# Kernel tuning notes

Hardware: AMD Instinct MI355X
Metric: run time of the kernel (lower is better)

The kernel has to match this reference:

```python
import jax, jax.numpy as jnp
from jax import lax
import numpy as np

H = 768          # BERT-base hidden size
NLAB = 2         # labelnum
T = NLAB + 2     # CRF tagset incl START/STOP (NCRF++ convention)
START = NLAB     # index 2
STOP = NLAB + 1  # index 3


def setup_inputs() -> dict:
    key = jax.random.key(0)
    ks = jax.random.split(key, 8)
    B, S1 = 64, 513  # S1 = 1 (CLS) + 512 content tokens
    emb = jax.random.normal(ks[0], (B, S1, H), dtype=jnp.float32)
    answer_seq_label = jax.random.randint(ks[1], (B, S1), 0, NLAB)
    IsQA = jax.random.randint(ks[2], (B,), 0, 2)
    fc2_W = jax.random.normal(ks[3], (2, H), dtype=jnp.float32) * 0.02
    fc2_b = jnp.zeros((2,), dtype=jnp.float32)
    crf_W = jax.random.normal(ks[4], (T, H), dtype=jnp.float32) * 0.02
    crf_b = jnp.zeros((T,), dtype=jnp.float32)
    transitions = jax.random.normal(ks[5], (T, T), dtype=jnp.float32) * 0.1
    return {"emb": emb, "answer_seq_label": answer_seq_label, "IsQA": IsQA,
            "fc2_W": fc2_W, "fc2_b": fc2_b, "crf_W": crf_W, "crf_b": crf_b,
            "transitions": transitions}


def _crf_log_partition(feats, trans):
    # feats [B,S,T]; linear-chain forward algorithm (log-sum-exp scan)
    alpha0 = feats[:, 0] + trans[START][None]           # [B,T]
    def step(alpha, feat_t):
        # alpha[b,prev] + trans[prev,cur] -> logsumexp over prev
        new = jax.nn.logsumexp(alpha[:, :, None] + trans[None], axis=1) + feat_t
        return new, None
    alpha, _ = lax.scan(step, alpha0, jnp.swapaxes(feats[:, 1:], 0, 1))
    return jax.nn.logsumexp(alpha + trans[:, STOP][None], axis=1)  # [B]


def _crf_gold_score(feats, tags, trans):
    # feats [B,S,T], tags [B,S]
    emit = jnp.take_along_axis(feats, tags[:, :, None], axis=2)[..., 0].sum(axis=1)
    tr = trans[tags[:, :-1], tags[:, 1:]].sum(axis=1)
    tr = tr + trans[START, tags[:, 0]] + trans[tags[:, -1], STOP]
    return emit + tr


def _crf_viterbi(feats, trans):
    # feats [B,S,T] -> best path [B,S]
    delta0 = feats[:, 0] + trans[START][None]
    def step(delta, feat_t):
        scores = delta[:, :, None] + trans[None]   # [B,prev,cur]
        bp = jnp.argmax(scores, axis=1)            # [B,T]
        return jnp.max(scores, axis=1) + feat_t, bp
    delta, bps = lax.scan(step, delta0, jnp.swapaxes(feats[:, 1:], 0, 1))  # bps [S-1,B,T]
    last_tag = jnp.argmax(delta + trans[:, STOP][None], axis=1)            # [B]
    def back(tag, bp_t):
        prev = jnp.take_along_axis(bp_t, tag[:, None], axis=1)[:, 0]
        return prev, prev
    _, path_prefix = lax.scan(back, last_tag, bps, reverse=True)           # [S-1,B]
    return jnp.concatenate([path_prefix, last_tag[None]], axis=0).T        # [B,S]


def reference(emb, answer_seq_label, IsQA, fc2_W, fc2_b, crf_W, crf_b, transitions):
    # CLS head + cross-entropy
    cls_emb = emb[:, 0]                              # [B,H]
    isqa_logits = cls_emb @ fc2_W.T + fc2_b          # [B,2]
    logp = jax.nn.log_softmax(isqa_logits, axis=-1)
    isqa_loss = -jnp.take_along_axis(logp, IsQA[:, None], axis=1).mean()
    isqa_pred = jnp.argmax(isqa_logits, axis=-1)[:, None]
    # CRF head (dropout = identity in eval); feats [B,S,T]
    feats = jnp.einsum('bsh,th->bst', emb[:, 1:], crf_W) + crf_b
    tags = answer_seq_label[:, 1:]
    Z = _crf_log_partition(feats, transitions)
    gold = _crf_gold_score(feats, tags, transitions)
    crf_loss = jnp.mean(Z - gold)
    crf_pred = _crf_viterbi(feats, transitions)
    return (isqa_pred, crf_pred, isqa_loss, crf_loss, tags, IsQA[:, None])
```

## Files before the change

kernel.cpp:

```cpp
#include <hip/hip_runtime.h>
#include <math.h>

#define B     64
#define S1    513
#define S     512
#define H     768
#define T     4
#define START 2
#define STOP  3

#define OUT_ISQA_PRED 0
#define OUT_CRF_PRED  64
#define OUT_ISQA_LOSS 32832
#define OUT_CRF_LOSS  32833
#define OUT_TAGS      32834
#define OUT_ISQA      65602

#define WS_FEATS  0
#define WS_LOGITS (B*S*T)
#define WS_ZG     (B*S*T + 2*B)
#define WS_CNT    (B*S*T + 3*B)
#define WS_FEATST 131280

template<int CTRL>
__device__ __forceinline__ float dppf(float x) {
    int v = __builtin_amdgcn_update_dpp(__builtin_bit_cast(int, x),
                                        __builtin_bit_cast(int, x),
                                        CTRL, 0xF, 0xF, false);
    return __builtin_bit_cast(float, v);
}
template<int CTRL>
__device__ __forceinline__ int dppi(int x) {
    return __builtin_amdgcn_update_dpp(x, x, CTRL, 0xF, 0xF, false);
}

__device__ __forceinline__ float lse4(float x0, float x1, float x2, float x3) {
    float m = fmaxf(fmaxf(x0, x1), fmaxf(x2, x3));
    return m + __logf(__expf(x0 - m) + __expf(x1 - m) +
                      __expf(x2 - m) + __expf(x3 - m));
}

__device__ __forceinline__ float wred(float a) {
    a += dppf<0xB1>(a); a += dppf<0x4E>(a);
    a += __shfl_xor(a, 4); a += __shfl_xor(a, 8);
    a += __shfl_xor(a, 16); a += __shfl_xor(a, 32);
    return a;
}

__device__ __forceinline__ float dot4(float4 e, float4 w) {
    return e.x * w.x + e.y * w.y + e.z * w.z + e.w * w.w;
}

__global__ __launch_bounds__(64) void feats_kernel(
    const float* __restrict__ emb,
    const float* __restrict__ crf_W, const float* __restrict__ crf_b,
    float* __restrict__ ws)
{
    if (blockIdx.x == 0 && threadIdx.x == 0)
        ((int*)ws)[WS_CNT] = 0;

    const int lane = threadIdx.x;
    const int r    = blockIdx.x * 64 + lane;
    const int b    = r >> 9;
    const int s    = (r & 511) + 1;

    const float4* __restrict__ src4 =
        (const float4*)emb + (size_t)(b * S1 + s) * (H / 4);
    const float4* __restrict__ W4 = (const float4*)crf_W;

    float a0 = 0.f, a1 = 0.f, a2 = 0.f, a3 = 0.f;
    #pragma unroll 8
    for (int k = 0; k < 192; ++k) {
        const float4 e  = src4[k];
        const float4 w0 = W4[0 * 192 + k];
        const float4 w1 = W4[1 * 192 + k];
        const float4 w2 = W4[2 * 192 + k];
        const float4 w3 = W4[3 * 192 + k];
        a0 += dot4(e, w0);
        a1 += dot4(e, w1);
        a2 += dot4(e, w2);
        a3 += dot4(e, w3);
    }

    const float v0 = a0 + crf_b[0];
    const float v1 = a1 + crf_b[1];
    const float v2 = a2 + crf_b[2];
    const float v3 = a3 + crf_b[3];

    float* __restrict__ fN = ws + WS_FEATS;
    float* __restrict__ fT = ws + WS_FEATST;
    ((float4*)fN)[b * S + (s - 1)] = make_float4(v0, v1, v2, v3);
    const int tb = b * 4 * S + (s - 1);
    fT[tb + 0 * S] = v0;
    fT[tb + 1 * S] = v1;
    fT[tb + 2 * S] = v2;
    fT[tb + 3 * S] = v3;
}

__device__ __forceinline__ unsigned int vstep(
    float& d, float fv,
    float tc0, float tc1, float tc2, float tc3, int sh8j)
{
    const float d0 = dppf<0x00>(d), d1 = dppf<0x55>(d);
    const float d2 = dppf<0xAA>(d), d3 = dppf<0xFF>(d);
    const float y0 = d0 + tc0, y1 = d1 + tc1;
    const float y2 = d2 + tc2, y3 = d3 + tc3;
    const float m01 = fmaxf(y0, y1), m23 = fmaxf(y2, y3);
    const int   i01 = (y1 > y0) ? 1 : 0;
    const int   i23 = (y3 > y2) ? 3 : 2;
    const int   bi  = (m23 > m01) ? i23 : i01;
    d = fmaxf(m01, m23) + fv;
    unsigned int mb = (unsigned int)bi << sh8j;
    unsigned int t1 = mb | (unsigned int)dppi<0xB1>((int)mb);
    return t1 | (unsigned int)dppi<0x4E>((int)t1);
}

__global__ __launch_bounds__(256) void crf_kernel(
    const int* __restrict__ ans, const int* __restrict__ isqa,
    const float* __restrict__ emb,
    const float* __restrict__ fc2_W, const float* __restrict__ fc2_b,
    const float* __restrict__ trans,
    float* __restrict__ ws, float* __restrict__ out)
{
    __shared__ float smemf[10784];
    __shared__ int isLast;
    const int tid = threadIdx.x;
    const int blk = blockIdx.x;

    if (blk < 64) {
        const int b = blk;
        float* sf  = smemf;
        float* C   = smemf + 2048;
        float* red = smemf + 3072;

        float tr[16];
        #pragma unroll
        for (int i = 0; i < 16; ++i) tr[i] = trans[i];

        {
            float4* sf4 = (float4*)sf;
            const float4* src4 = (const float4*)(ws + WS_FEATS) + b * 512;
            sf4[tid] = src4[tid];
            sf4[tid + 256] = src4[tid + 256];
        }

        if (tid < 128) {
            const int wv   = tid >> 6;
            const int lane = tid & 63;
            const float4* e4 = (const float4*)emb + (size_t)b * S1 * (H / 4);
            const float4* w4 = (const float4*)fc2_W + wv * 192;
            float acc = 0.f;
            #pragma unroll
            for (int k = 0; k < 3; ++k) {
                const float4 e = e4[lane + 64 * k];
                const float4 w = w4[lane + 64 * k];
                acc += dot4(e, w);
            }
            acc = wred(acc);
            if (lane == 0) {
                ws[WS_LOGITS + 2 * b + wv] = acc + fc2_b[wv];
                __threadfence();
            }
        }
        __syncthreads();

        float g = 0.f;
        #pragma unroll
        for (int u = 0; u < 2; ++u) {
            const int t   = 2 * tid + u;
            const int tag = ans[b * S1 + 1 + t];
            out[OUT_TAGS + b * S + t] = (float)tag;
            g += sf[t * 4 + tag];
            g += (t == 0) ? tr[START * 4 + tag] : tr[ans[b * S1 + t] * 4 + tag];
            if (t == S - 1) g += tr[tag * 4 + STOP];
        }
        #pragma unroll
        for (int m = 32; m; m >>= 1) g += __shfl_xor(g, m);
        if ((tid & 63) == 0) red[tid >> 6] = g;

        const int c  = tid >> 2;
        const int jr = tid & 3;
        const int t0 = c ? 8 * c : 1;
        float rl[4];
        #pragma unroll
        for (int i = 0; i < 4; ++i) rl[i] = tr[jr * 4 + i] + sf[t0 * 4 + i];
        for (int t = t0 + 1; t <= 8 * c + 7; ++t) {
            const float f0 = sf[t*4+0], f1 = sf[t*4+1], f2 = sf[t*4+2], f3 = sf[t*4+3];
            float nr[4];
            #pragma unroll
            for (int i = 0; i < 4; ++i)
                nr[i] = lse4(rl[0] + tr[0*4+i], rl[1] + tr[1*4+i],
                             rl[2] + tr[2*4+i], rl[3] + tr[3*4+i]);
            rl[0] = nr[0] + f0; rl[1] = nr[1] + f1;
            rl[2] = nr[2] + f2; rl[3] = nr[3] + f3;
        }
        ((float4*)C)[c * 4 + jr] = make_float4(rl[0], rl[1], rl[2], rl[3]);
        __syncthreads();

        for (int d = 1; d <= 32; d <<= 1) {
            const int cs = (c >= d) ? (c - d) : c;
            float4 ar = ((float4*)C)[cs * 4 + jr];
            float4 b0 = ((float4*)C)[c * 4 + 0];
            float4 b1 = ((float4*)C)[c * 4 + 1];
            float4 b2 = ((float4*)C)[c * 4 + 2];
            float4 b3 = ((float4*)C)[c * 4 + 3];
            __syncthreads();
            if (c >= d) {
                float4 nr;
                nr.x = lse4(ar.x + b0.x, ar.y + b1.x, ar.z + b2.x, ar.w + b3.x);
                nr.y = lse4(ar.x + b0.y, ar.y + b1.y, ar.z + b2.y, ar.w + b3.y);
                nr.z = lse4(ar.x + b0.z, ar.y + b1.z, ar.z + b2.z, ar.w + b3.z);
                nr.w = lse4(ar.x + b0.w, ar.y + b1.w, ar.z + b2.w, ar.w + b3.w);
                ((float4*)C)[c * 4 + jr] = nr;
            }
            __syncthreads();
        }

        if (tid == 0) {
            const float gold = red[0] + red[1] + red[2] + red[3];
            float a0k[4];
            #pragma unroll
            for (int k = 0; k < 4; ++k) a0k[k] = sf[k] + tr[START * 4 + k];
            const float* P = C + 63 * 16;
            float aN[4];
            #pragma unroll
            for (int i = 0; i < 4; ++i)
                aN[i] = lse4(a0k[0] + P[0*4+i], a0k[1] + P[1*4+i],
                             a0k[2] + P[2*4+i], a0k[3] + P[3*4+i]);
            const float Z = lse4(aN[0] + tr[0*4+STOP], aN[1] + tr[1*4+STOP],
                                 aN[2] + tr[2*4+STOP], aN[3] + tr[3*4+STOP]);
            ws[WS_ZG + b] = Z - gold;
            out[OUT_ISQA + b] = (float)isqa[b];
            __threadfence();
            const int old = atomicAdd((int*)ws + WS_CNT, 1);
            isLast = (old == 63);
        }
        __syncthreads();

        if (isLast && tid < 64) {
            __threadfence();
            const float zg = ws[WS_ZG + tid];
            const float l0 = ws[WS_LOGITS + tid * 2 + 0];
            const float l1 = ws[WS_LOGITS + tid * 2 + 1];
            const float m  = fmaxf(l0, l1);
            const float lse = m + __logf(__expf(l0 - m) + __expf(l1 - m));
            const int   y   = isqa[tid];
            const float li  = lse - (y ? l1 : l0);
            float s1 = zg, s2 = li;
            #pragma unroll
            for (int d = 32; d; d >>= 1) {
                s1 += __shfl_xor(s1, d);
                s2 += __shfl_xor(s2, d);
            }
            out[OUT_ISQA_PRED + tid] = (l1 > l0) ? 1.0f : 0.0f;
            if (tid == 0) {
                out[OUT_CRF_LOSS]  = s1 * (1.0f / 64.0f);
                out[OUT_ISQA_LOSS] = s2 * (1.0f / 64.0f);
            }
        }
    } else {
        const int bv = blk - 64;
        float* sfT = smemf;
        unsigned int* bpw = (unsigned int*)(smemf + 8208);
        {
            float4* d4 = (float4*)sfT;
            const float4* s4 = (const float4*)(ws + WS_FEATST) + bv * 4 * 512;
            #pragma unroll
            for (int n = 0; n < 8; ++n) d4[tid + 256 * n] = s4[tid + 256 * n];
        }
        if (tid < 4) ((float4*)(sfT + 8192))[tid & 3] =
            make_float4(0.f, 0.f, 0.f, 0.f);
        __syncthreads();

        const int w    = tid >> 6;
        const int lane = tid & 63;
        const int j    = lane & 3;
        const int b    = bv * 4 + w;
        const int sh8j = 8 * j;

        const float tc0 = trans[0*4+j], tc1 = trans[1*4+j];
        const float tc2 = trans[2*4+j], tc3 = trans[3*4+j];
        const float tSj = trans[START*4+j];
        const float tjs = trans[j*4 + STOP];

        const float4* colT4 = (const float4*)(sfT + w * 2048 + j * 512);
        uint4* bpq = (uint4*)(bpw + w * 512);

        float4 A  = colT4[0];
        float4 Bq = colT4[1];
        float4 B2 = colT4[2];
        float d = A.x + tSj;
        {
            const unsigned int W1 = vstep(d, A.y, tc0, tc1, tc2, tc3, sh8j);
            const unsigned int W2 = vstep(d, A.z, tc0, tc1, tc2, tc3, sh8j);
            const unsigned int W3 = vstep(d, A.w, tc0, tc1, tc2, tc3, sh8j);
            if (lane == 0) bpq[0] = make_uint4(0x03020100u, W1, W2, W3);
        }
        for (int g = 1; g < 128; ++g) {
            const float4 Cq = colT4[g + 2];
            const unsigned int W0 = vstep(d, Bq.x, tc0, tc1, tc2, tc3, sh8j);
            const unsigned int W1 = vstep(d, Bq.y, tc0, tc1, tc2, tc3, sh8j);
            const unsigned int W2 = vstep(d, Bq.z, tc0, tc1, tc2, tc3, sh8j);
            const unsigned int W3 = vstep(d, Bq.w, tc0, tc1, tc2, tc3, sh8j);
            if (lane == 0) bpq[g] = make_uint4(W0, W1, W2, W3);
            Bq = B2; B2 = Cq;
        }

        const float vj = d + tjs;
        const float z0 = dppf<0x00>(vj), z1 = dppf<0x55>(vj);
        const float z2 = dppf<0xAA>(vj), z3 = dppf<0xFF>(vj);
        float m01 = z0; unsigned int i01 = 0;
        if (z1 > m01) { m01 = z1; i01 = 1; }
        float m23 = z2; unsigned int i23 = 2;
        if (z3 > m23) { m23 = z3; i23 = 3; }
        const unsigned int lt = (m23 > m01) ? i23 : i01;

        __syncthreads();

        const uint4 wv0 = bpq[lane * 2 + 0];
        const uint4 wv1 = bpq[lane * 2 + 1];
        unsigned int wk[8] = {wv0.x, wv0.y, wv0.z, wv0.w, wv1.x, wv1.y, wv1.z, wv1.w};
        unsigned int G = wk[7];
        #pragma unroll
        for (int k = 6; k >= 0; --k)
            G = __builtin_amdgcn_perm(0u, wk[k], G);
        unsigned int Sm = G;
        #pragma unroll
        for (int dd = 1; dd < 64; dd <<= 1) {
            const int srcl = lane + dd;
            const unsigned int oth = __shfl(Sm, (srcl < 64) ? srcl : 63);
            if (srcl < 64) Sm = __builtin_amdgcn_perm(0u, Sm, oth);
        }
        unsigned int emap = __shfl(Sm, (lane < 63) ? lane + 1 : 63);
        if (lane == 63) emap = 0x03020100u;
        unsigned int cur = (emap >> (8 * lt)) & 3u;

        float tg[8];
        tg[7] = (float)cur;
        #pragma unroll
        for (int k = 7; k >= 1; --k) {
            cur = (wk[k] >> (8 * cur)) & 3u;
            tg[k - 1] = (float)cur;
        }
        float4* op = (float4*)(out + OUT_CRF_PRED + b * S + lane * 8);
        op[0] = make_float4(tg[0], tg[1], tg[2], tg[3]);
        op[1] = make_float4(tg[4], tg[5], tg[6], tg[7]);
    }
}

extern "C" void kernel_launch(void* const* d_in, const int* in_sizes, int n_in,
                              void* d_out, int out_size, void* d_ws, size_t ws_size,
                              hipStream_t stream)
{
    const float* emb    = (const float*)d_in[0];
    const int*   ans    = (const int*)d_in[1];
    const int*   isqa   = (const int*)d_in[2];
    const float* fc2_W  = (const float*)d_in[3];
    const float* fc2_b  = (const float*)d_in[4];
    const float* crf_W  = (const float*)d_in[5];
    const float* crf_b  = (const float*)d_in[6];
    const float* trans  = (const float*)d_in[7];
    float* out = (float*)d_out;
    float* ws  = (float*)d_ws;

    feats_kernel<<<512, 64, 0, stream>>>(emb, crf_W, crf_b, ws);
    crf_kernel<<<80, 256, 0, stream>>>(ans, isqa, emb, fc2_W, fc2_b, trans, ws, out);
}
```

Baseline: 224.3 us.

## Stage embedding tiles through LDS with coalesced loads and split-K reduction

Restructures the feats projection kernel. Before, each thread streamed a whole 768-float row alone, giving strided, uncoalesced global loads. Now 256 threads cooperatively load 64-row by 16-float4 chunks into double-buffered, padded LDS, with crf_W cached in LDS. Each row's dot products are split across four thread groups and combined through shared memory. This aims for coalesced HBM reads and more memory-level parallelism, at the cost of extra LDS traffic and a barrier per chunk.

```diff
diff --git a/kernel.cpp b/kernel.cpp
--- a/kernel.cpp
+++ b/kernel.cpp
@@ -22,6 +22,11 @@
 #define WS_CNT    (B*S*T + 3*B)
 #define WS_FEATST 131280
 
+#define RB   64
+#define KC   16
+#define NC   12
+#define RS   17
+
 template<int CTRL>
 __device__ __forceinline__ float dppf(float x) {
     int v = __builtin_amdgcn_update_dpp(__builtin_bit_cast(int, x),
@@ -51,50 +56,96 @@
     return e.x * w.x + e.y * w.y + e.z * w.z + e.w * w.w;
 }
 
-__global__ __launch_bounds__(64) void feats_kernel(
+__global__ __launch_bounds__(256) void feats_kernel(
     const float* __restrict__ emb,
     const float* __restrict__ crf_W, const float* __restrict__ crf_b,
     float* __restrict__ ws)
 {
-    if (blockIdx.x == 0 && threadIdx.x == 0)
-        ((int*)ws)[WS_CNT] = 0;
-
-    const int lane = threadIdx.x;
-    const int r    = blockIdx.x * 64 + lane;
-    const int b    = r >> 9;
-    const int s    = (r & 511) + 1;
-
-    const float4* __restrict__ src4 =
-        (const float4*)emb + (size_t)(b * S1 + s) * (H / 4);
-    const float4* __restrict__ W4 = (const float4*)crf_W;
+    __shared__ float4 wlds[4 * 192];
+    __shared__ float4 buf[2][RB * RS];
+    __shared__ float4 red[3][RB];
+
+    const int tid = threadIdx.x;
+    const int blk = blockIdx.x;
+    if (blk == 0 && tid == 0) ((int*)ws)[WS_CNT] = 0;
+
+    {
+        const float4* W4 = (const float4*)crf_W;
+        wlds[tid]       = W4[tid];
+        wlds[tid + 256] = W4[tid + 256];
+        wlds[tid + 512] = W4[tid + 512];
+    }
+
+    const int s16 = tid & 15;
+    const int r16 = tid >> 4;
+    const float4* __restrict__ emb4 = (const float4*)emb;
+    size_t sbase[4];
+    #pragma unroll
+    for (int p = 0; p < 4; ++p) {
+        const int row = blk * RB + r16 + 16 * p;
+        const int b   = row >> 9;
+        const int s   = (row & 511) + 1;
+        sbase[p] = (size_t)(b * S1 + s) * (H / 4) + s16;
+    }
+
+    const int rb = tid & 63;
+    const int q  = tid >> 6;
+
+    #pragma unroll
+    for (int p = 0; p < 4; ++p)
+        buf[0][(r16 + 16 * p) * RS + s16] = emb4[sbase[p]];
+    __syncthreads();
 
     float a0 = 0.f, a1 = 0.f, a2 = 0.f, a3 = 0.f;
-    #pragma unroll 8
-    for (int k = 0; k < 192; ++k) {
-        const float4 e  = src4[k];
-        const float4 w0 = W4[0 * 192 + k];
-        const float4 w1 = W4[1 * 192 + k];
-        const float4 w2 = W4[2 * 192 + k];
-        const float4 w3 = W4[3 * 192 + k];
-        a0 += dot4(e, w0);
-        a1 += dot4(e, w1);
-        a2 += dot4(e, w2);
-        a3 += dot4(e, w3);
+    int pb = 0;
+    for (int c = 0; c < NC; ++c) {
+        if (c + 1 < NC) {
+            #pragma unroll
+            for (int p = 0; p < 4; ++p)
+                buf[pb ^ 1][(r16 + 16 * p) * RS + s16] =
+                    emb4[sbase[p] + (size_t)(c + 1) * KC];
+        }
+        const float4* __restrict__ myrow = &buf[pb][rb * RS + q * 4];
+        const float4* __restrict__ w0 = &wlds[0 * 192 + c * 16 + q * 4];
+        const float4* __restrict__ w1 = &wlds[1 * 192 + c * 16 + q * 4];
+        const float4* __restrict__ w2 = &wlds[2 * 192 + c * 16 + q * 4];
+        const float4* __restrict__ w3 = &wlds[3 * 192 + c * 16 + q * 4];
+        #pragma unroll
+        for (int i = 0; i < 4; ++i) {
+            const float4 e = myrow[i];
+            a0 += dot4(e, w0[i]);
+            a1 += dot4(e, w1[i]);
+            a2 += dot4(e, w2[i]);
+            a3 += dot4(e, w3[i]);
+        }
+        __syncthreads();
+        pb ^= 1;
     }
 
-    const float v0 = a0 + crf_b[0];
-    const float v1 = a1 + crf_b[1];
-    const float v2 = a2 + crf_b[2];
-    const float v3 = a3 + crf_b[3];
-
-    float* __restrict__ fN = ws + WS_FEATS;
-    float* __restrict__ fT = ws + WS_FEATST;
-    ((float4*)fN)[b * S + (s - 1)] = make_float4(v0, v1, v2, v3);
-    const int tb = b * 4 * S + (s - 1);
-    fT[tb + 0 * S] = v0;
-    fT[tb + 1 * S] = v1;
-    fT[tb + 2 * S] = v2;
-    fT[tb + 3 * S] = v3;
+    if (q != 0) red[q - 1][rb] = make_float4(a0, a1, a2, a3);
+    __syncthreads();
+    if (q == 0) {
+        #pragma unroll
+        for (int k = 0; k < 3; ++k) {
+            const float4 r = red[k][rb];
+            a0 += r.x; a1 += r.y; a2 += r.z; a3 += r.w;
+        }
+        const int row = blk * RB + rb;
+        const int b   = row >> 9;
+        const int s   = (row & 511) + 1;
+        const float v0 = a0 + crf_b[0];
+        const float v1 = a1 + crf_b[1];
+        const float v2 = a2 + crf_b[2];
+        const float v3 = a3 + crf_b[3];
+        float* __restrict__ fN = ws + WS_FEATS;
+        float* __restrict__ fT = ws + WS_FEATST;
+        ((float4*)fN)[b * S + (s - 1)] = make_float4(v0, v1, v2, v3);
+        const int tb = b * 4 * S + (s - 1);
+        fT[tb + 0 * S] = v0;
+        fT[tb + 1 * S] = v1;
+        fT[tb + 2 * S] = v2;
+        fT[tb + 3 * S] = v3;
+    }
 }
 
 __device__ __forceinline__ unsigned int vstep(
@@ -363,6 +414,6 @@
     float* out = (float*)d_out;
     float* ws  = (float*)d_ws;
 
-    feats_kernel<<<512, 64, 0, stream>>>(emb, crf_W, crf_b, ws);
+    feats_kernel<<<512, 256, 0, stream>>>(emb, crf_W, crf_b, ws);
     crf_kernel<<<80, 256, 0, stream>>>(ans, isqa, emb, fc2_W, fc2_b, trans, ws, out);
 }
```

Result: faster. 198.9 us (-11.3%).
